# Kernel optimization log

Hardware: AMD Instinct MI355X
Metric: run time of the kernel (lower is better)

Reference implementation:

```python
import jax, jax.numpy as jnp
import numpy as np

C = 128
GROUPS = 8
EPS = 1e-5


def setup_inputs() -> dict:
    key = jax.random.key(0)
    ks = jax.random.split(key, 7)
    x = jax.random.normal(ks[0], (8, C, 256, 256), dtype=jnp.float32)
    gn_w = jax.random.normal(ks[1], (C,), dtype=jnp.float32) * 0.02 + 1.0
    gn_b = jax.random.normal(ks[2], (C,), dtype=jnp.float32) * 0.02
    w1 = jax.random.normal(ks[3], (C, C), dtype=jnp.float32) * (1.0 / np.sqrt(C))
    b1 = jax.random.normal(ks[4], (C,), dtype=jnp.float32) * 0.02
    w2 = jax.random.normal(ks[5], (C, C), dtype=jnp.float32) * (1.0 / np.sqrt(C))
    b2 = jax.random.normal(ks[6], (C,), dtype=jnp.float32) * 0.02
    return {"x": x, "gn_w": gn_w, "gn_b": gn_b, "w1": w1, "b1": b1, "w2": w2, "b2": b2}


def reference(x, gn_w, gn_b, w1, b1, w2, b2):
    # fft2 -> ifft2(..).real round-trip (faithful to original; numerically ~identity)
    x_ifft = jnp.fft.ifft2(jnp.fft.fft2(x, axes=(-2, -1)), axes=(-2, -1)).real.astype(x.dtype)

    # GroupNorm over (C//G, H, W) per group
    B, Ch, H, W = x_ifft.shape
    g = x_ifft.reshape(B, GROUPS, Ch // GROUPS, H, W)
    mean = g.mean(axis=(2, 3, 4), keepdims=True)
    var = g.var(axis=(2, 3, 4), keepdims=True)
    xn = ((g - mean) * jax.lax.rsqrt(var + EPS)).reshape(B, Ch, H, W)
    xn = xn * gn_w[None, :, None, None] + gn_b[None, :, None, None]

    # 1x1 conv -> ReLU -> 1x1 conv (as channel GEMMs)
    h = jnp.einsum('oc,bchw->bohw', w1, xn) + b1[None, :, None, None]
    h = jax.nn.relu(h)
    ffn = jnp.einsum('oc,bchw->bohw', w2, h) + b2[None, :, None, None]
    return x_ifft + ffn
```

## Files before the change

### kernel.cpp

```cpp
#include <hip/hip_runtime.h>

typedef __attribute__((ext_vector_type(8))) short s16x8;
typedef __attribute__((ext_vector_type(4))) float f32x4;
typedef unsigned int u32;

#define CCH 128

__device__ __forceinline__ ushort f2bf(float f) {
  uint u = __float_as_uint(f);
  u += 0x7fffu + ((u >> 16) & 1u);
  return (ushort)(u >> 16);
}
__device__ __forceinline__ float bf2f(ushort u) {
  return __uint_as_float(((uint)u) << 16);
}

__device__ __forceinline__ int swz(int row, int col) {
  return (row << 7) | (col ^ ((row & 7) << 3));
}

__device__ __forceinline__ void gll16(const void* g, void* l) {
  __builtin_amdgcn_global_load_lds((const __attribute__((address_space(1))) u32*)g,
                                   (__attribute__((address_space(3))) u32*)l, 16, 0, 0);
}

__global__ __launch_bounds__(256) void pass1(const float* __restrict__ x,
                                             ushort* __restrict__ xb,
                                             float2* __restrict__ partials) {
  __shared__ ushort sT[128 * CCH];
  __shared__ float wsa[4][4], wsb[4][4];
  const int t = threadIdx.x;
  const int blk = ((blockIdx.x & 7) << 9) | (blockIdx.x >> 3);
  const int b = blk >> 9;
  const int p0 = (blk & 511) << 7;
  const int wv = t >> 6, lane = t & 63;
  const int px4 = (t & 31) * 4;
  const int c8 = t >> 5;

  float sa[4], sq[4];
#pragma unroll
  for (int i = 0; i < 4; ++i) { sa[i] = 0.f; sq[i] = 0.f; }

  const float* xbase = x + (((size_t)b * CCH) << 16) + p0;
#pragma unroll
  for (int i = 0; i < 4; ++i) {
    const int ch = i * 32 + c8 * 4;
    float4 v[4];
#pragma unroll
    for (int j = 0; j < 4; ++j)
      v[j] = *(const float4*)(xbase + (((size_t)(ch + j)) << 16) + px4);
#pragma unroll
    for (int j = 0; j < 4; ++j) {
      sa[i] += v[j].x + v[j].y + v[j].z + v[j].w;
      sq[i] += v[j].x * v[j].x + v[j].y * v[j].y + v[j].z * v[j].z + v[j].w * v[j].w;
    }
    const int c4 = i * 8 + c8;
#pragma unroll
    for (int k = 0; k < 4; ++k) {
      const int row = px4 + k;
      const int gs = c4 ^ (((row >> 3) & 15) << 1);
      ushort4 pk;
      pk.x = f2bf(((const float*)&v[0])[k]);
      pk.y = f2bf(((const float*)&v[1])[k]);
      pk.z = f2bf(((const float*)&v[2])[k]);
      pk.w = f2bf(((const float*)&v[3])[k]);
      *(ushort4*)&sT[row * CCH + gs * 4] = pk;
    }
  }
#pragma unroll
  for (int i = 0; i < 4; ++i) {
    float a = sa[i], q = sq[i];
#pragma unroll
    for (int off = 32; off > 0; off >>= 1) {
      a += __shfl_down(a, off);
      q += __shfl_down(q, off);
    }
    if (lane == 0) { wsa[wv][i] = a; wsb[wv][i] = q; }
  }
  __syncthreads();
  if (t < 8) {
    const int g = t;
    const int w0 = (g & 1) * 2, ii = g >> 1;
    partials[blk * 8 + g] =
        (float2){wsa[w0][ii] + wsa[w0 + 1][ii], wsb[w0][ii] + wsb[w0 + 1][ii]};
  }
  const int g = t & 15, pr = t >> 4;
  ushort* dst = xb + ((size_t)blk << 14);
#pragma unroll
  for (int s = 0; s < 8; ++s) {
    const int row = s * 16 + pr;
    const int sidx = row * CCH + (((2 * g) ^ (((row >> 3) & 15) << 1)) * 4);
    const int didx = row * CCH + ((g ^ (row & 7)) * 8);
    *(s16x8*)&dst[didx] = *(const s16x8*)&sT[sidx];
  }
}

__global__ void stats_finalize2(const float2* __restrict__ partials,
                                const float* __restrict__ gn_w,
                                const float* __restrict__ gn_b,
                                float* __restrict__ scale, float* __restrict__ shift) {
  const int t = threadIdx.x;
  const int b = t >> 3, g = t & 7;
  float s1 = 0.f, s2 = 0.f;
  for (int c = 0; c < 512; ++c) {
    float2 p = partials[(b * 512 + c) * 8 + g];
    s1 += p.x;
    s2 += p.y;
  }
  const float invN = 1.0f / 1048576.0f;
  const float mean = s1 * invN;
  const float var = s2 * invN - mean * mean;
  const float rstd = rsqrtf(var + 1e-5f);
  for (int i = 0; i < 16; ++i) {
    const int c = g * 16 + i;
    const float sc = rstd * gn_w[c];
    scale[b * CCH + c] = sc;
    shift[b * CCH + c] = gn_b[c] - mean * sc;
  }
}

__global__ __launch_bounds__(256) void prep_w2(const float* __restrict__ w2,
                                               ushort* __restrict__ w2b) {
  int i = blockIdx.x * 256 + threadIdx.x;
  float4 a = ((const float4*)w2)[i];
  ushort4 o;
  o.x = f2bf(a.x); o.y = f2bf(a.y); o.z = f2bf(a.z); o.w = f2bf(a.w);
  ((ushort4*)w2b)[i] = o;
}

__global__ __launch_bounds__(128) void fold_w1(const float* __restrict__ w1,
                                               const float* __restrict__ b1,
                                               const float* __restrict__ scale,
                                               const float* __restrict__ shift,
                                               ushort* __restrict__ W1b,
                                               float* __restrict__ c1) {
  const int b = blockIdx.x >> 7, o = blockIdx.x & 127, c = threadIdx.x;
  const float wv = w1[o * CCH + c];
  W1b[(b << 14) + o * CCH + c] = f2bf(wv * scale[b * CCH + c]);
  float s = wv * shift[b * CCH + c];
#pragma unroll
  for (int off = 32; off > 0; off >>= 1) s += __shfl_down(s, off);
  __shared__ float tmp[2];
  if ((threadIdx.x & 63) == 0) tmp[threadIdx.x >> 6] = s;
  __syncthreads();
  if (threadIdx.x == 0) c1[(b << 7) + o] = tmp[0] + tmp[1] + b1[o];
}

#define NT 8
__global__ __launch_bounds__(256) void mlp_pipe(
    const ushort* __restrict__ xb, const ushort* __restrict__ W1b,
    const ushort* __restrict__ w2b, const float* __restrict__ c1,
    const float* __restrict__ b2, float* __restrict__ out) {
  __shared__ ushort sB[2][128 * CCH];
  const int t = threadIdx.x, lane = t & 63, wv = t >> 6;
  const int fl = lane & 15, fh = lane >> 4;
  const int blk = ((blockIdx.x & 7) << 6) | (blockIdx.x >> 3);
  const int gt0 = blk * NT;
  const int b = gt0 >> 9;
  const ushort* w1p = W1b + (b << 14);
  const float* c1b = c1 + (b << 7);

  {
    const char* s0 = (const char*)xb + ((size_t)gt0 << 15) + wv * 8192 + lane * 16;
    ushort* l0 = &sB[0][wv * 4096];
#pragma unroll
    for (int i = 0; i < 8; ++i) gll16(s0 + i * 1024, l0 + i * 512);
  }

#pragma unroll 1
  for (int it = 0; it < NT; ++it) {
    const int cur = it & 1;
    const int gt = gt0 + it;
    if (it + 1 < NT) {
      const char* s0 = (const char*)xb + ((size_t)(gt + 1) << 15) + wv * 8192 + lane * 16;
      ushort* l0 = &sB[cur ^ 1][wv * 4096];
#pragma unroll
      for (int i = 0; i < 8; ++i) gll16(s0 + i * 1024, l0 + i * 512);
      __builtin_amdgcn_sched_barrier(0);
      asm volatile("s_waitcnt vmcnt(8)" ::: "memory");
    } else {
      asm volatile("s_waitcnt vmcnt(0)" ::: "memory");
    }
    __builtin_amdgcn_sched_barrier(0);
    __builtin_amdgcn_s_barrier();
    __builtin_amdgcn_sched_barrier(0);

    ushort* sb = &sB[cur][0];

    f32x4 acc[2][8];
#pragma unroll
    for (int f = 0; f < 2; ++f)
#pragma unroll
      for (int j = 0; j < 8; ++j) acc[f][j] = (f32x4){0.f, 0.f, 0.f, 0.f};
#pragma unroll
    for (int k0 = 0; k0 < 128; k0 += 32) {
      const int kb = k0 + fh * 8;
      const s16x8 a0 = *(const s16x8*)(w1p + (wv * 32 + fl) * CCH + kb);
      const s16x8 a1 = *(const s16x8*)(w1p + (wv * 32 + 16 + fl) * CCH + kb);
#pragma unroll
      for (int j = 0; j < 8; ++j) {
        const s16x8 bf = *(const s16x8*)&sb[swz(j * 16 + fl, kb)];
        acc[0][j] = __builtin_amdgcn_mfma_f32_16x16x32_bf16(a0, bf, acc[0][j], 0, 0, 0);
        acc[1][j] = __builtin_amdgcn_mfma_f32_16x16x32_bf16(a1, bf, acc[1][j], 0, 0, 0);
      }
    }
    asm volatile("s_waitcnt lgkmcnt(0)" ::: "memory");
    __builtin_amdgcn_sched_barrier(0);
    __builtin_amdgcn_s_barrier();
    __builtin_amdgcn_sched_barrier(0);

    ushort4 rx[2][8];
#pragma unroll
    for (int f = 0; f < 2; ++f) {
      const int ob = wv * 32 + f * 16 + fh * 4;
      const float4 cc = *(const float4*)(c1b + ob);
#pragma unroll
      for (int j = 0; j < 8; ++j) {
        ushort* p = &sb[swz(j * 16 + fl, ob)];
        rx[f][j] = *(const ushort4*)p;
        ushort4 pk;
        pk.x = f2bf(fmaxf(acc[f][j][0] + cc.x, 0.f));
        pk.y = f2bf(fmaxf(acc[f][j][1] + cc.y, 0.f));
        pk.z = f2bf(fmaxf(acc[f][j][2] + cc.z, 0.f));
        pk.w = f2bf(fmaxf(acc[f][j][3] + cc.w, 0.f));
        *(ushort4*)p = pk;
      }
    }
    asm volatile("s_waitcnt lgkmcnt(0)" ::: "memory");
    __builtin_amdgcn_sched_barrier(0);
    __builtin_amdgcn_s_barrier();
    __builtin_amdgcn_sched_barrier(0);

    f32x4 acc2[2][8];
#pragma unroll
    for (int f = 0; f < 2; ++f)
#pragma unroll
      for (int j = 0; j < 8; ++j) acc2[f][j] = (f32x4){0.f, 0.f, 0.f, 0.f};
#pragma unroll
    for (int k0 = 0; k0 < 128; k0 += 32) {
      const int kb = k0 + fh * 8;
      const s16x8 a0 = *(const s16x8*)(w2b + (wv * 32 + fl) * CCH + kb);
      const s16x8 a1 = *(const s16x8*)(w2b + (wv * 32 + 16 + fl) * CCH + kb);
#pragma unroll
      for (int j = 0; j < 8; ++j) {
        const s16x8 bf = *(const s16x8*)&sb[swz(j * 16 + fl, kb)];
        acc2[0][j] = __builtin_amdgcn_mfma_f32_16x16x32_bf16(a0, bf, acc2[0][j], 0, 0, 0);
        acc2[1][j] = __builtin_amdgcn_mfma_f32_16x16x32_bf16(a1, bf, acc2[1][j], 0, 0, 0);
      }
    }
    asm volatile("s_waitcnt lgkmcnt(0)" ::: "memory");
    __builtin_amdgcn_sched_barrier(0);
    __builtin_amdgcn_s_barrier();
    __builtin_amdgcn_sched_barrier(0);

    float* sF = (float*)sb;
    const int p0 = (gt & 511) << 7;
    const int rowbase = wv * 16;
#pragma unroll
    for (int f = 0; f < 2; ++f) {
      const int ob = wv * 32 + f * 16 + fh * 4;
      const float4 bb = *(const float4*)(b2 + ob);
#pragma unroll
      for (int j = 0; j < 8; ++j) {
        const int rb = (rowbase + fh * 4) * 128 + j * 16 + fl;
        sF[rb]       = acc2[f][j][0] + bb.x + bf2f(rx[f][j].x);
        sF[rb + 128] = acc2[f][j][1] + bb.y + bf2f(rx[f][j].y);
        sF[rb + 256] = acc2[f][j][2] + bb.z + bf2f(rx[f][j].z);
        sF[rb + 384] = acc2[f][j][3] + bb.w + bf2f(rx[f][j].w);
      }
#pragma unroll
      for (int i = 0; i < 16; ++i) {
        const float2 v = *(const float2*)&sF[(rowbase + i) * 128 + lane * 2];
        const int ch = wv * 32 + f * 16 + i;
        *(float2*)(out + (((size_t)(b * CCH + ch)) << 16) + p0 + lane * 2) = v;
      }
    }
    asm volatile("s_waitcnt lgkmcnt(0)" ::: "memory");
    __builtin_amdgcn_sched_barrier(0);
    __builtin_amdgcn_s_barrier();
    __builtin_amdgcn_sched_barrier(0);
  }
}

extern "C" void kernel_launch(void* const* d_in, const int* in_sizes, int n_in,
                              void* d_out, int out_size, void* d_ws, size_t ws_size,
                              hipStream_t stream) {
  const float* x    = (const float*)d_in[0];
  const float* gn_w = (const float*)d_in[1];
  const float* gn_b = (const float*)d_in[2];
  const float* w1   = (const float*)d_in[3];
  const float* b1   = (const float*)d_in[4];
  const float* w2   = (const float*)d_in[5];
  const float* b2   = (const float*)d_in[6];
  float* out = (float*)d_out;
  char* ws = (char*)d_ws;

  const size_t XB = (size_t)8 * 65536 * CCH * 2;
  ushort* xbuf  = (ushort*)ws;
  float2* parts = (float2*)(ws + XB);
  ushort* W1b   = (ushort*)(ws + XB);
  float* scale  = (float*)(ws + XB + 262144);
  float* shift  = (float*)(ws + XB + 266240);
  ushort* w2b   = (ushort*)(ws + XB + 270336);
  float* c1     = (float*)(ws + XB + 303104);

  hipLaunchKernelGGL(pass1, dim3(4096), dim3(256), 0, stream, x, xbuf, parts);
  hipLaunchKernelGGL(stats_finalize2, dim3(1), dim3(64), 0, stream, parts, gn_w, gn_b, scale, shift);
  hipLaunchKernelGGL(fold_w1, dim3(1024), dim3(128), 0, stream, w1, b1, scale, shift, W1b, c1);
  hipLaunchKernelGGL(prep_w2, dim3(16), dim3(256), 0, stream, w2, w2b);
  hipLaunchKernelGGL(mlp_pipe, dim3(512), dim3(256), 0, stream, xbuf, W1b, w2b, c1, b2, out);
}
```

Baseline: 260.5 us.

## Replace persistent double-buffered MLP kernel with small 64-pixel tile blocks

Replaces the persistent 512-block, 256-thread MLP kernel that looped over 8 double-buffered 128-pixel tiles with 8192 independent 128-thread blocks, each handling 64 pixels using a 17KB LDS tile. The goal is higher occupancy (launch bounds of 4 blocks per SIMD group) so that latency is hidden through concurrency instead of explicit prefetch pipelining. The residual is now re-read from global memory rather than kept in registers, and the workspace layout is moved so W1b no longer aliases the partials buffer. This adds redundant global residual reads and drops the explicit load/compute overlap.

```diff
diff --git a/kernel.cpp b/kernel.cpp
--- a/kernel.cpp
+++ b/kernel.cpp
@@ -13,10 +13,6 @@
 }
 __device__ __forceinline__ float bf2f(ushort u) {
   return __uint_as_float(((uint)u) << 16);
-}
-
-__device__ __forceinline__ int swz(int row, int col) {
-  return (row << 7) | (col ^ ((row & 7) << 3));
 }
 
 __device__ __forceinline__ void gll16(const void* g, void* l) {
@@ -146,139 +142,144 @@
   if (threadIdx.x == 0) c1[(b << 7) + o] = tmp[0] + tmp[1] + b1[o];
 }
 
-#define NT 8
-__global__ __launch_bounds__(256) void mlp_pipe(
+__global__ __launch_bounds__(128, 4) void mlp64(
     const ushort* __restrict__ xb, const ushort* __restrict__ W1b,
     const ushort* __restrict__ w2b, const float* __restrict__ c1,
     const float* __restrict__ b2, float* __restrict__ out) {
-  __shared__ ushort sB[2][128 * CCH];
+  __shared__ float sF[64 * 68];
+  ushort* sB = (ushort*)sF;
   const int t = threadIdx.x, lane = t & 63, wv = t >> 6;
   const int fl = lane & 15, fh = lane >> 4;
-  const int blk = ((blockIdx.x & 7) << 6) | (blockIdx.x >> 3);
-  const int gt0 = blk * NT;
-  const int b = gt0 >> 9;
+  const int blk = ((blockIdx.x & 7) << 10) | (blockIdx.x >> 3);
+  const int b = blk >> 10;
+  const int p0 = (blk & 1023) << 6;
   const ushort* w1p = W1b + (b << 14);
   const float* c1b = c1 + (b << 7);
+  const char* img = (const char*)xb + ((size_t)(blk >> 1) << 15) + ((size_t)(blk & 1) << 14);
 
   {
-    const char* s0 = (const char*)xb + ((size_t)gt0 << 15) + wv * 8192 + lane * 16;
-    ushort* l0 = &sB[0][wv * 4096];
-#pragma unroll
-    for (int i = 0; i < 8; ++i) gll16(s0 + i * 1024, l0 + i * 512);
-  }
-
-#pragma unroll 1
-  for (int it = 0; it < NT; ++it) {
-    const int cur = it & 1;
-    const int gt = gt0 + it;
-    if (it + 1 < NT) {
-      const char* s0 = (const char*)xb + ((size_t)(gt + 1) << 15) + wv * 8192 + lane * 16;
-      ushort* l0 = &sB[cur ^ 1][wv * 4096];
-#pragma unroll
-      for (int i = 0; i < 8; ++i) gll16(s0 + i * 1024, l0 + i * 512);
-      __builtin_amdgcn_sched_barrier(0);
-      asm volatile("s_waitcnt vmcnt(8)" ::: "memory");
-    } else {
-      asm volatile("s_waitcnt vmcnt(0)" ::: "memory");
-    }
-    __builtin_amdgcn_sched_barrier(0);
-    __builtin_amdgcn_s_barrier();
-    __builtin_amdgcn_sched_barrier(0);
-
-    ushort* sb = &sB[cur][0];
-
-    f32x4 acc[2][8];
+    const char* src = img + wv * 8192 + lane * 16;
+    ushort* dstl = &sB[wv * 4096];
+#pragma unroll
+    for (int i = 0; i < 8; ++i) gll16(src + i * 1024, dstl + i * 512);
+  }
+  __builtin_amdgcn_sched_barrier(0);
+  asm volatile("s_waitcnt vmcnt(0)" ::: "memory");
+  __builtin_amdgcn_sched_barrier(0);
+  __builtin_amdgcn_s_barrier();
+  __builtin_amdgcn_sched_barrier(0);
+
+  f32x4 acc[4][4];
+#pragma unroll
+  for (int j = 0; j < 4; ++j)
+#pragma unroll
+    for (int p = 0; p < 4; ++p) acc[j][p] = (f32x4){0.f, 0.f, 0.f, 0.f};
+
+#pragma unroll
+  for (int k0 = 0; k0 < 4; ++k0) {
+    const int kb = k0 * 32 + fh * 8;
+    const int gb = k0 * 4 + fh;
+    s16x8 bt[4];
+#pragma unroll
+    for (int p = 0; p < 4; ++p) {
+      const int px = p * 16 + fl;
+      bt[p] = *(const s16x8*)&sB[px * CCH + ((gb ^ (px & 7)) << 3)];
+    }
+#pragma unroll
+    for (int j = 0; j < 4; ++j) {
+      const s16x8 a = *(const s16x8*)(w1p + (wv * 64 + j * 16 + fl) * CCH + kb);
+#pragma unroll
+      for (int p = 0; p < 4; ++p)
+        acc[j][p] = __builtin_amdgcn_mfma_f32_16x16x32_bf16(a, bt[p], acc[j][p], 0, 0, 0);
+    }
+  }
+  asm volatile("s_waitcnt lgkmcnt(0)" ::: "memory");
+  __builtin_amdgcn_sched_barrier(0);
+  __builtin_amdgcn_s_barrier();
+  __builtin_amdgcn_sched_barrier(0);
+
+#pragma unroll
+  for (int j = 0; j < 4; ++j) {
+    const int hc0 = wv * 64 + j * 16 + fh * 4;
+    const float4 cc = *(const float4*)(c1b + hc0);
+    const int g = hc0 >> 3, e = hc0 & 7;
+#pragma unroll
+    for (int p = 0; p < 4; ++p) {
+      const int px = p * 16 + fl;
+      ushort4 pk;
+      pk.x = f2bf(fmaxf(acc[j][p][0] + cc.x, 0.f));
+      pk.y = f2bf(fmaxf(acc[j][p][1] + cc.y, 0.f));
+      pk.z = f2bf(fmaxf(acc[j][p][2] + cc.z, 0.f));
+      pk.w = f2bf(fmaxf(acc[j][p][3] + cc.w, 0.f));
+      *(ushort4*)&sB[px * CCH + ((g ^ (px & 7)) << 3) + e] = pk;
+    }
+  }
+  asm volatile("s_waitcnt lgkmcnt(0)" ::: "memory");
+  __builtin_amdgcn_sched_barrier(0);
+  __builtin_amdgcn_s_barrier();
+  __builtin_amdgcn_sched_barrier(0);
+
+  f32x4 acc2[2][2][4];
+#pragma unroll
+  for (int f = 0; f < 2; ++f)
+#pragma unroll
+    for (int e = 0; e < 2; ++e)
+#pragma unroll
+      for (int p = 0; p < 4; ++p) acc2[f][e][p] = (f32x4){0.f, 0.f, 0.f, 0.f};
+
+#pragma unroll
+  for (int k0 = 0; k0 < 4; ++k0) {
+    const int kb = k0 * 32 + fh * 8;
+    const int gb = k0 * 4 + fh;
+    s16x8 bt[4];
+#pragma unroll
+    for (int p = 0; p < 4; ++p) {
+      const int px = p * 16 + fl;
+      bt[p] = *(const s16x8*)&sB[px * CCH + ((gb ^ (px & 7)) << 3)];
+    }
 #pragma unroll
     for (int f = 0; f < 2; ++f)
 #pragma unroll
-      for (int j = 0; j < 8; ++j) acc[f][j] = (f32x4){0.f, 0.f, 0.f, 0.f};
-#pragma unroll
-    for (int k0 = 0; k0 < 128; k0 += 32) {
-      const int kb = k0 + fh * 8;
-      const s16x8 a0 = *(const s16x8*)(w1p + (wv * 32 + fl) * CCH + kb);
-      const s16x8 a1 = *(const s16x8*)(w1p + (wv * 32 + 16 + fl) * CCH + kb);
-#pragma unroll
-      for (int j = 0; j < 8; ++j) {
-        const s16x8 bf = *(const s16x8*)&sb[swz(j * 16 + fl, kb)];
-        acc[0][j] = __builtin_amdgcn_mfma_f32_16x16x32_bf16(a0, bf, acc[0][j], 0, 0, 0);
-        acc[1][j] = __builtin_amdgcn_mfma_f32_16x16x32_bf16(a1, bf, acc[1][j], 0, 0, 0);
+      for (int e = 0; e < 2; ++e) {
+        const s16x8 a = *(const s16x8*)(w2b + (f * 64 + wv * 32 + e * 16 + fl) * CCH + kb);
+#pragma unroll
+        for (int p = 0; p < 4; ++p)
+          acc2[f][e][p] =
+              __builtin_amdgcn_mfma_f32_16x16x32_bf16(a, bt[p], acc2[f][e][p], 0, 0, 0);
+      }
+  }
+  asm volatile("s_waitcnt lgkmcnt(0)" ::: "memory");
+  __builtin_amdgcn_sched_barrier(0);
+  __builtin_amdgcn_s_barrier();
+  __builtin_amdgcn_sched_barrier(0);
+
+#pragma unroll
+  for (int f = 0; f < 2; ++f) {
+#pragma unroll
+    for (int e = 0; e < 2; ++e) {
+      const int oc0 = f * 64 + wv * 32 + e * 16 + fh * 4;
+      const float4 bbv = *(const float4*)(b2 + oc0);
+      const int rloc = wv * 32 + e * 16 + fh * 4;
+      const int gr = ((oc0 >> 3) << 4) , er = (oc0 & 7) * 2;
+#pragma unroll
+      for (int p = 0; p < 4; ++p) {
+        const int px = p * 16 + fl;
+        const ushort4 rx =
+            *(const ushort4*)(img + px * 256 + (((oc0 >> 3) ^ (px & 7)) << 4) + er);
+        sF[(rloc + 0) * 68 + px] = acc2[f][e][p][0] + bbv.x + bf2f(rx.x);
+        sF[(rloc + 1) * 68 + px] = acc2[f][e][p][1] + bbv.y + bf2f(rx.y);
+        sF[(rloc + 2) * 68 + px] = acc2[f][e][p][2] + bbv.z + bf2f(rx.z);
+        sF[(rloc + 3) * 68 + px] = acc2[f][e][p][3] + bbv.w + bf2f(rx.w);
       }
     }
     asm volatile("s_waitcnt lgkmcnt(0)" ::: "memory");
     __builtin_amdgcn_sched_barrier(0);
-    __builtin_amdgcn_s_barrier();
-    __builtin_amdgcn_sched_barrier(0);
-
-    ushort4 rx[2][8];
-#pragma unroll
-    for (int f = 0; f < 2; ++f) {
-      const int ob = wv * 32 + f * 16 + fh * 4;
-      const float4 cc = *(const float4*)(c1b + ob);
-#pragma unroll
-      for (int j = 0; j < 8; ++j) {
-        ushort* p = &sb[swz(j * 16 + fl, ob)];
-        rx[f][j] = *(const ushort4*)p;
-        ushort4 pk;
-        pk.x = f2bf(fmaxf(acc[f][j][0] + cc.x, 0.f));
-        pk.y = f2bf(fmaxf(acc[f][j][1] + cc.y, 0.f));
-        pk.z = f2bf(fmaxf(acc[f][j][2] + cc.z, 0.f));
-        pk.w = f2bf(fmaxf(acc[f][j][3] + cc.w, 0.f));
-        *(ushort4*)p = pk;
-      }
-    }
-    asm volatile("s_waitcnt lgkmcnt(0)" ::: "memory");
-    __builtin_amdgcn_sched_barrier(0);
-    __builtin_amdgcn_s_barrier();
-    __builtin_amdgcn_sched_barrier(0);
-
-    f32x4 acc2[2][8];
-#pragma unroll
-    for (int f = 0; f < 2; ++f)
-#pragma unroll
-      for (int j = 0; j < 8; ++j) acc2[f][j] = (f32x4){0.f, 0.f, 0.f, 0.f};
-#pragma unroll
-    for (int k0 = 0; k0 < 128; k0 += 32) {
-      const int kb = k0 + fh * 8;
-      const s16x8 a0 = *(const s16x8*)(w2b + (wv * 32 + fl) * CCH + kb);
-      const s16x8 a1 = *(const s16x8*)(w2b + (wv * 32 + 16 + fl) * CCH + kb);
-#pragma unroll
-      for (int j = 0; j < 8; ++j) {
-        const s16x8 bf = *(const s16x8*)&sb[swz(j * 16 + fl, kb)];
-        acc2[0][j] = __builtin_amdgcn_mfma_f32_16x16x32_bf16(a0, bf, acc2[0][j], 0, 0, 0);
-        acc2[1][j] = __builtin_amdgcn_mfma_f32_16x16x32_bf16(a1, bf, acc2[1][j], 0, 0, 0);
-      }
-    }
-    asm volatile("s_waitcnt lgkmcnt(0)" ::: "memory");
-    __builtin_amdgcn_sched_barrier(0);
-    __builtin_amdgcn_s_barrier();
-    __builtin_amdgcn_sched_barrier(0);
-
-    float* sF = (float*)sb;
-    const int p0 = (gt & 511) << 7;
-    const int rowbase = wv * 16;
-#pragma unroll
-    for (int f = 0; f < 2; ++f) {
-      const int ob = wv * 32 + f * 16 + fh * 4;
-      const float4 bb = *(const float4*)(b2 + ob);
-#pragma unroll
-      for (int j = 0; j < 8; ++j) {
-        const int rb = (rowbase + fh * 4) * 128 + j * 16 + fl;
-        sF[rb]       = acc2[f][j][0] + bb.x + bf2f(rx[f][j].x);
-        sF[rb + 128] = acc2[f][j][1] + bb.y + bf2f(rx[f][j].y);
-        sF[rb + 256] = acc2[f][j][2] + bb.z + bf2f(rx[f][j].z);
-        sF[rb + 384] = acc2[f][j][3] + bb.w + bf2f(rx[f][j].w);
-      }
-#pragma unroll
-      for (int i = 0; i < 16; ++i) {
-        const float2 v = *(const float2*)&sF[(rowbase + i) * 128 + lane * 2];
-        const int ch = wv * 32 + f * 16 + i;
-        *(float2*)(out + (((size_t)(b * CCH + ch)) << 16) + p0 + lane * 2) = v;
-      }
-    }
-    asm volatile("s_waitcnt lgkmcnt(0)" ::: "memory");
-    __builtin_amdgcn_sched_barrier(0);
-    __builtin_amdgcn_s_barrier();
-    __builtin_amdgcn_sched_barrier(0);
+#pragma unroll
+    for (int i = 0; i < 16; ++i) {
+      const int rloc = wv * 32 + i * 2 + (lane >> 5);
+      const float2 v = *(const float2*)&sF[rloc * 68 + (lane & 31) * 2];
+      *(float2*)(out + (((size_t)(b * CCH + f * 64 + rloc)) << 16) + p0 + (lane & 31) * 2) = v;
+    }
   }
 }
 
@@ -298,15 +299,15 @@
   const size_t XB = (size_t)8 * 65536 * CCH * 2;
   ushort* xbuf  = (ushort*)ws;
   float2* parts = (float2*)(ws + XB);
-  ushort* W1b   = (ushort*)(ws + XB);
   float* scale  = (float*)(ws + XB + 262144);
   float* shift  = (float*)(ws + XB + 266240);
   ushort* w2b   = (ushort*)(ws + XB + 270336);
-  float* c1     = (float*)(ws + XB + 303104);
+  ushort* W1b   = (ushort*)(ws + XB + 303104);
+  float* c1     = (float*)(ws + XB + 565248);
 
   hipLaunchKernelGGL(pass1, dim3(4096), dim3(256), 0, stream, x, xbuf, parts);
   hipLaunchKernelGGL(stats_finalize2, dim3(1), dim3(64), 0, stream, parts, gn_w, gn_b, scale, shift);
   hipLaunchKernelGGL(fold_w1, dim3(1024), dim3(128), 0, stream, w1, b1, scale, shift, W1b, c1);
   hipLaunchKernelGGL(prep_w2, dim3(16), dim3(256), 0, stream, w2, w2b);
-  hipLaunchKernelGGL(mlp_pipe, dim3(512), dim3(256), 0, stream, xbuf, W1b, w2b, c1, b2, out);
-}
+  hipLaunchKernelGGL(mlp64, dim3(8192), dim3(128), 0, stream, xbuf, W1b, w2b, c1, b2, out);
+}
```

Result: slower. 273.7 us (+5.1%).
